# Kernel tuning notes

Hardware: AMD Instinct MI355X
Metric: run time of the kernel (lower is better)

The kernel has to match this reference:

```python
import jax, jax.numpy as jnp
import numpy as np

N, C, D = 131072, 1024, 128

def setup_inputs() -> dict:
    key = jax.random.key(0)
    kx, kw = jax.random.split(key)
    x = jax.random.normal(kx, (N, D), dtype=jnp.float32)
    prototypes = jax.random.normal(kw, (C, D), dtype=jnp.float32)
    return {"x": x, "prototypes": prototypes}

def reference(x, prototypes):
    # Pairwise squared Euclidean distance: dist[n, c] = sum_d (x[n,d] - w[c,d])^2
    x_sq = jnp.sum(x * x, axis=-1, keepdims=True)            # [N, 1]
    w_sq = jnp.sum(prototypes * prototypes, axis=-1)          # [C]
    cross = jnp.einsum('nd,cd->nc', x, prototypes)            # [N, C]
    return x_sq + w_sq[None, :] - 2.0 * cross                 # [N, C]
```

## Files before the change

### kernel.cpp

```cpp
#include <hip/hip_runtime.h>
#include <cstdint>
#include <cstddef>

#define D_DIM 128

typedef __attribute__((ext_vector_type(8))) __bf16 bf16x8;
typedef __attribute__((ext_vector_type(4))) float f32x4;

__device__ __forceinline__ unsigned short f2bf(float f) {
    unsigned u = __builtin_bit_cast(unsigned, f);
    u += 0x7FFFu + ((u >> 16) & 1u);
    return (unsigned short)(u >> 16);
}
__device__ __forceinline__ float bf2f(unsigned short h) {
    unsigned u = ((unsigned)h) << 16;
    return __builtin_bit_cast(float, u);
}

__global__ __launch_bounds__(256) void prep_kernel(
    const float* __restrict__ x, const float* __restrict__ w,
    unsigned short* __restrict__ xb, unsigned short* __restrict__ wb,
    float* __restrict__ xsq, float* __restrict__ wsq,
    int n_rows_x, int n_rows_w)
{
    const int wave = threadIdx.x >> 6;
    const int lane = threadIdx.x & 63;
    const int half = lane >> 5;
    const int l32  = lane & 31;
    int row = blockIdx.x * 8 + wave * 2 + half;

    const float* src; unsigned short* dst; float* nrm; int r = row;
    if (row < n_rows_x) { src = x; dst = xb; nrm = xsq; }
    else {
        r = row - n_rows_x;
        if (r >= n_rows_w) return;
        src = w; dst = wb; nrm = wsq;
    }

    const float4 v = reinterpret_cast<const float4*>(src + (size_t)r * D_DIM)[l32];
    unsigned short b0 = f2bf(v.x), b1 = f2bf(v.y), b2 = f2bf(v.z), b3 = f2bf(v.w);
    float f0 = bf2f(b0), f1 = bf2f(b1), f2 = bf2f(b2), f3 = bf2f(b3);
    uint2 pack;
    pack.x = (unsigned)b0 | ((unsigned)b1 << 16);
    pack.y = (unsigned)b2 | ((unsigned)b3 << 16);
    reinterpret_cast<uint2*>(dst + (size_t)r * D_DIM)[l32] = pack;

    float s = f0 * f0 + f1 * f1 + f2 * f2 + f3 * f3;
    #pragma unroll
    for (int off = 16; off > 0; off >>= 1) s += __shfl_xor(s, off, 64);
    if (l32 == 0) nrm[r] = s;
}

__global__ __launch_bounds__(256, 2) void rbf_gemm(
    const unsigned short* __restrict__ xb, const unsigned short* __restrict__ wb,
    const float* __restrict__ xsq, const float* __restrict__ wsq,
    float* __restrict__ out, int C_total, int tiles_c, int tiles_m)
{
    int ty, tx;
    {
        const int bid = blockIdx.x;
        if ((tiles_m & 7) == 0) {
            const int xcd = bid & 7;
            const int i   = bid >> 3;
            const int iy  = i / tiles_c;
            ty = xcd * (tiles_m >> 3) + iy;
            tx = i - iy * tiles_c;
        } else {
            ty = bid / tiles_c;
            tx = bid - ty * tiles_c;
        }
    }

    const int lane   = threadIdx.x & 63;
    const int wave   = threadIdx.x >> 6;
    const int lane16 = lane & 15;
    const int quad   = lane >> 4;
    const int wm = (wave & 1) * 64;
    const int wc = (wave >> 1) * 64;

    const long m0 = (long)ty * 128;
    const long c0 = (long)tx * 128;

    const unsigned short* abase = xb + (size_t)(m0 + wm + lane16) * D_DIM + quad * 8;
    const unsigned short* bbase = wb + (size_t)(c0 + wc + lane16) * D_DIM + quad * 8;

    f32x4 acc[4][4];
    #pragma unroll
    for (int i = 0; i < 4; ++i)
        #pragma unroll
        for (int j = 0; j < 4; ++j)
            acc[i][j] = (f32x4){0.f, 0.f, 0.f, 0.f};

    #pragma unroll
    for (int kk = 0; kk < D_DIM; kk += 32) {
        bf16x8 a[4], b[4];
        #pragma unroll
        for (int mt = 0; mt < 4; ++mt)
            a[mt] = *reinterpret_cast<const bf16x8*>(abase + (size_t)mt * 16 * D_DIM + kk);
        #pragma unroll
        for (int ct = 0; ct < 4; ++ct)
            b[ct] = *reinterpret_cast<const bf16x8*>(bbase + (size_t)ct * 16 * D_DIM + kk);
        #pragma unroll
        for (int ct = 0; ct < 4; ++ct)
            #pragma unroll
            for (int mt = 0; mt < 4; ++mt)
                acc[ct][mt] = __builtin_amdgcn_mfma_f32_16x16x32_bf16(
                    b[ct], a[mt], acc[ct][mt], 0, 0, 0);
    }

    float xsv[4];
    #pragma unroll
    for (int mt = 0; mt < 4; ++mt)
        xsv[mt] = xsq[m0 + wm + mt * 16 + lane16];
    f32x4 wsv[4];
    #pragma unroll
    for (int ct = 0; ct < 4; ++ct)
        wsv[ct] = *reinterpret_cast<const f32x4*>(wsq + c0 + wc + ct * 16 + quad * 4);

    #pragma unroll
    for (int mt = 0; mt < 4; ++mt) {
        const long m = m0 + wm + mt * 16 + lane16;
        float* orow = out + m * (long)C_total + c0 + wc + quad * 4;
        #pragma unroll
        for (int ct = 0; ct < 4; ++ct) {
            f32x4 v;
            #pragma unroll
            for (int r = 0; r < 4; ++r)
                v[r] = xsv[mt] + wsv[ct][r] - 2.0f * acc[ct][mt][r];
            __builtin_nontemporal_store(v, reinterpret_cast<f32x4*>(orow + ct * 16));
        }
    }
}

extern "C" void kernel_launch(void* const* d_in, const int* in_sizes, int n_in,
                              void* d_out, int out_size, void* d_ws, size_t ws_size,
                              hipStream_t stream) {
    const float* x = (const float*)d_in[0];
    const float* w = (const float*)d_in[1];
    float* out = (float*)d_out;

    const int N = in_sizes[0] / D_DIM;
    const int C = in_sizes[1] / D_DIM;

    unsigned short* xb = (unsigned short*)d_ws;
    unsigned short* wb = xb + (size_t)N * D_DIM;
    float* xsq = (float*)(wb + (size_t)C * D_DIM);
    float* wsq = xsq + N;

    const int rows = N + C;
    prep_kernel<<<(rows + 7) / 8, 256, 0, stream>>>(x, w, xb, wb, xsq, wsq, N, C);

    const int tiles_m = N / 128;
    const int tiles_c = C / 128;
    rbf_gemm<<<dim3(tiles_m * tiles_c), 256, 0, stream>>>(
        xb, wb, xsq, wsq, out, C, tiles_c, tiles_m);
}
```

Baseline: 631.7 us.

## Fuse bf16 conversion and norm computation into the GEMM kernel

```diff
diff --git a/kernel.cpp b/kernel.cpp
--- a/kernel.cpp
+++ b/kernel.cpp
@@ -7,53 +7,8 @@
 typedef __attribute__((ext_vector_type(8))) __bf16 bf16x8;
 typedef __attribute__((ext_vector_type(4))) float f32x4;
 
-__device__ __forceinline__ unsigned short f2bf(float f) {
-    unsigned u = __builtin_bit_cast(unsigned, f);
-    u += 0x7FFFu + ((u >> 16) & 1u);
-    return (unsigned short)(u >> 16);
-}
-__device__ __forceinline__ float bf2f(unsigned short h) {
-    unsigned u = ((unsigned)h) << 16;
-    return __builtin_bit_cast(float, u);
-}
-
-__global__ __launch_bounds__(256) void prep_kernel(
+__global__ __launch_bounds__(256, 2) void rbf_fused(
     const float* __restrict__ x, const float* __restrict__ w,
-    unsigned short* __restrict__ xb, unsigned short* __restrict__ wb,
-    float* __restrict__ xsq, float* __restrict__ wsq,
-    int n_rows_x, int n_rows_w)
-{
-    const int wave = threadIdx.x >> 6;
-    const int lane = threadIdx.x & 63;
-    const int half = lane >> 5;
-    const int l32  = lane & 31;
-    int row = blockIdx.x * 8 + wave * 2 + half;
-
-    const float* src; unsigned short* dst; float* nrm; int r = row;
-    if (row < n_rows_x) { src = x; dst = xb; nrm = xsq; }
-    else {
-        r = row - n_rows_x;
-        if (r >= n_rows_w) return;
-        src = w; dst = wb; nrm = wsq;
-    }
-
-    const float4 v = reinterpret_cast<const float4*>(src + (size_t)r * D_DIM)[l32];
-    unsigned short b0 = f2bf(v.x), b1 = f2bf(v.y), b2 = f2bf(v.z), b3 = f2bf(v.w);
-    float f0 = bf2f(b0), f1 = bf2f(b1), f2 = bf2f(b2), f3 = bf2f(b3);
-    uint2 pack;
-    pack.x = (unsigned)b0 | ((unsigned)b1 << 16);
-    pack.y = (unsigned)b2 | ((unsigned)b3 << 16);
-    reinterpret_cast<uint2*>(dst + (size_t)r * D_DIM)[l32] = pack;
-
-    float s = f0 * f0 + f1 * f1 + f2 * f2 + f3 * f3;
-    #pragma unroll
-    for (int off = 16; off > 0; off >>= 1) s += __shfl_xor(s, off, 64);
-    if (l32 == 0) nrm[r] = s;
-}
-
-__global__ __launch_bounds__(256, 2) void rbf_gemm(
-    const unsigned short* __restrict__ xb, const unsigned short* __restrict__ wb,
-    const float* __restrict__ xsq, const float* __restrict__ wsq,
     float* __restrict__ out, int C_total, int tiles_c, int tiles_m)
 {
     int ty, tx;
@@ -81,8 +36,8 @@
     const long m0 = (long)ty * 128;
     const long c0 = (long)tx * 128;
 
-    const unsigned short* abase = xb + (size_t)(m0 + wm + lane16) * D_DIM + quad * 8;
-    const unsigned short* bbase = wb + (size_t)(c0 + wc + lane16) * D_DIM + quad * 8;
+    const float* aptr = x + (size_t)(m0 + wm + lane16) * D_DIM + quad * 8;
+    const float* bptr = w + (size_t)(c0 + wc + lane16) * D_DIM + quad * 8;
 
     f32x4 acc[4][4];
     #pragma unroll
@@ -91,31 +46,76 @@
         for (int j = 0; j < 4; ++j)
             acc[i][j] = (f32x4){0.f, 0.f, 0.f, 0.f};
 
+    float sa[4] = {0.f, 0.f, 0.f, 0.f};
+    float sb[4] = {0.f, 0.f, 0.f, 0.f};
+
+#define LOADC(AF, BF, KC) do {                                              \
+        _Pragma("unroll")                                                   \
+        for (int t = 0; t < 4; ++t) {                                       \
+            const float* pa = aptr + (size_t)t * 16 * D_DIM + (KC) * 32;    \
+            AF[t][0] = *reinterpret_cast<const float4*>(pa);                \
+            AF[t][1] = *reinterpret_cast<const float4*>(pa + 4);            \
+            const float* pb = bptr + (size_t)t * 16 * D_DIM + (KC) * 32;    \
+            BF[t][0] = *reinterpret_cast<const float4*>(pb);                \
+            BF[t][1] = *reinterpret_cast<const float4*>(pb + 4);            \
+        }                                                                   \
+    } while (0)
+
+#define CVT8(DST, LO, HI) do {                                              \
+        DST[0] = (__bf16)(LO).x; DST[1] = (__bf16)(LO).y;                   \
+        DST[2] = (__bf16)(LO).z; DST[3] = (__bf16)(LO).w;                   \
+        DST[4] = (__bf16)(HI).x; DST[5] = (__bf16)(HI).y;                   \
+        DST[6] = (__bf16)(HI).z; DST[7] = (__bf16)(HI).w;                   \
+    } while (0)
+
+#define PROCESS(AF, BF) do {                                                \
+        bf16x8 a8[4], b8[4];                                                \
+        _Pragma("unroll")                                                   \
+        for (int t = 0; t < 4; ++t) {                                       \
+            float4 lo = AF[t][0], hi = AF[t][1];                            \
+            sa[t] += lo.x*lo.x + lo.y*lo.y + lo.z*lo.z + lo.w*lo.w          \
+                   + hi.x*hi.x + hi.y*hi.y + hi.z*hi.z + hi.w*hi.w;         \
+            CVT8(a8[t], lo, hi);                                            \
+            lo = BF[t][0]; hi = BF[t][1];                                   \
+            sb[t] += lo.x*lo.x + lo.y*lo.y + lo.z*lo.z + lo.w*lo.w          \
+                   + hi.x*hi.x + hi.y*hi.y + hi.z*hi.z + hi.w*hi.w;         \
+            CVT8(b8[t], lo, hi);                                            \
+        }                                                                   \
+        _Pragma("unroll")                                                   \
+        for (int ct = 0; ct < 4; ++ct)                                      \
+            _Pragma("unroll")                                               \
+            for (int mt = 0; mt < 4; ++mt)                                  \
+                acc[ct][mt] = __builtin_amdgcn_mfma_f32_16x16x32_bf16(      \
+                    b8[ct], a8[mt], acc[ct][mt], 0, 0, 0);                  \
+    } while (0)
+
+    float4 A0[4][2], B0[4][2], A1[4][2], B1[4][2];
+    LOADC(A0, B0, 0);
+    LOADC(A1, B1, 1);
+    PROCESS(A0, B0);
+    LOADC(A0, B0, 2);
+    PROCESS(A1, B1);
+    LOADC(A1, B1, 3);
+    PROCESS(A0, B0);
+    PROCESS(A1, B1);
+
+#undef LOADC
+#undef CVT8
+#undef PROCESS
+
     #pragma unroll
-    for (int kk = 0; kk < D_DIM; kk += 32) {
-        bf16x8 a[4], b[4];
-        #pragma unroll
-        for (int mt = 0; mt < 4; ++mt)
-            a[mt] = *reinterpret_cast<const bf16x8*>(abase + (size_t)mt * 16 * D_DIM + kk);
-        #pragma unroll
-        for (int ct = 0; ct < 4; ++ct)
-            b[ct] = *reinterpret_cast<const bf16x8*>(bbase + (size_t)ct * 16 * D_DIM + kk);
-        #pragma unroll
-        for (int ct = 0; ct < 4; ++ct)
-            #pragma unroll
-            for (int mt = 0; mt < 4; ++mt)
-                acc[ct][mt] = __builtin_amdgcn_mfma_f32_16x16x32_bf16(
-                    b[ct], a[mt], acc[ct][mt], 0, 0, 0);
+    for (int t = 0; t < 4; ++t) {
+        sa[t] += __shfl_xor(sa[t], 16, 64);
+        sa[t] += __shfl_xor(sa[t], 32, 64);
+        sb[t] += __shfl_xor(sb[t], 16, 64);
+        sb[t] += __shfl_xor(sb[t], 32, 64);
     }
-
-    float xsv[4];
-    #pragma unroll
-    for (int mt = 0; mt < 4; ++mt)
-        xsv[mt] = xsq[m0 + wm + mt * 16 + lane16];
     f32x4 wsv[4];
     #pragma unroll
     for (int ct = 0; ct < 4; ++ct)
-        wsv[ct] = *reinterpret_cast<const f32x4*>(wsq + c0 + wc + ct * 16 + quad * 4);
+        #pragma unroll
+        for (int r = 0; r < 4; ++r)
+            wsv[ct][r] = __shfl(sb[ct], quad * 4 + r, 16);
 
     #pragma unroll
     for (int mt = 0; mt < 4; ++mt) {
@@ -126,7 +126,7 @@
             f32x4 v;
             #pragma unroll
             for (int r = 0; r < 4; ++r)
-                v[r] = xsv[mt] + wsv[ct][r] - 2.0f * acc[ct][mt][r];
+                v[r] = sa[mt] + wsv[ct][r] - 2.0f * acc[ct][mt][r];
             __builtin_nontemporal_store(v, reinterpret_cast<f32x4*>(orow + ct * 16));
         }
     }
@@ -142,16 +142,8 @@
     const int N = in_sizes[0] / D_DIM;
     const int C = in_sizes[1] / D_DIM;
 
-    unsigned short* xb = (unsigned short*)d_ws;
-    unsigned short* wb = xb + (size_t)N * D_DIM;
-    float* xsq = (float*)(wb + (size_t)C * D_DIM);
-    float* wsq = xsq + N;
-
-    const int rows = N + C;
-    prep_kernel<<<(rows + 7) / 8, 256, 0, stream>>>(x, w, xb, wb, xsq, wsq, N, C);
-
     const int tiles_m = N / 128;
     const int tiles_c = C / 128;
-    rbf_gemm<<<dim3(tiles_m * tiles_c), 256, 0, stream>>>(
-        xb, wb, xsq, wsq, out, C, tiles_c, tiles_m);
+    rbf_fused<<<dim3(tiles_m * tiles_c), 256, 0, stream>>>(
+        x, w, out, C, tiles_c, tiles_m);
 }
```

Result: slower. 815.2 us (+29.1%).
